# Optimization experiments

Hardware: AMD Instinct MI355X
Metric: run time of the kernel (lower is better)

The kernel has to match this reference:

```python
import jax, jax.numpy as jnp
import numpy as np

B, N, C_IN, C_H, C_OUT, R, X_DIM = 32, 256, 64, 128, 128, 5, 1024
NEG = -9e15

def _leaky(x, s=0.2):
    return jnp.where(x >= 0, x, s * x)

def gat_layer(atoms, mask, W, b, a):
    # atoms: (B,n,c_in), mask: (B,n,n,R) bool, W: (c_in, R*c), b: (R*c,), a: (R, 2c)
    bs, n, _ = atoms.shape
    c = a.shape[1] // 2
    h = (atoms @ W + b).reshape(bs, n, R, c)            # (B,n,R,c)
    src = jnp.einsum('bnrc,rc->bnr', h, a[:, :c])       # a . h_i part
    dst = jnp.einsum('bnrc,rc->bnr', h, a[:, c:])       # a . h_j part
    logits = _leaky(src[:, :, None, :] + dst[:, None, :, :])  # (B,i,j,R)
    masked = jnp.where(mask, logits, NEG)
    probs = jax.nn.softmax(masked.reshape(bs, n, n * R), axis=2).reshape(bs, n, n, R)
    return jnp.einsum('bijr,bjrc->bic', probs, h)       # (B,n,c)

def setup_inputs() -> dict:
    key = jax.random.key(0)
    ks = jax.random.split(key, 16)
    def p(k, shape, fan):
        return jax.random.normal(k, shape, jnp.float32) * (1.414 / np.sqrt(fan))
    inp = {
        'x': jax.random.normal(ks[0], (B, X_DIM), jnp.float32),
        'y_atoms': jax.random.normal(ks[1], (B, N, C_IN), jnp.float32),
        'y_bonds': jax.random.randint(ks[2], (B, N, N, R), 0, 2, jnp.int32),
        'W1': p(ks[3], (C_IN, R * C_H), C_IN), 'b1': jnp.zeros((R * C_H,), jnp.float32),
        'a1': p(ks[4], (R, 2 * C_H), 2 * C_H),
        'W2': p(ks[5], (C_H, R * C_H), C_H), 'b2': jnp.zeros((R * C_H,), jnp.float32),
        'a2': p(ks[6], (R, 2 * C_H), 2 * C_H),
        'W3': p(ks[7], (C_H, R * C_OUT), C_H), 'b3': jnp.zeros((R * C_OUT,), jnp.float32),
        'a3': p(ks[8], (R, 2 * C_OUT), 2 * C_OUT),
        'We1': p(ks[9], (2 * C_OUT + X_DIM, 256), 2 * C_OUT + X_DIM), 'be1': jnp.zeros((256,), jnp.float32),
        'We2': p(ks[10], (256, 32), 256), 'be2': jnp.zeros((32,), jnp.float32),
        'We3': p(ks[11], (32, 1), 32), 'be3': jnp.zeros((1,), jnp.float32),
    }
    return inp

def reference(x, y_atoms, y_bonds, W1, b1, a1, W2, b2, a2, W3, b3, a3,
              We1, be1, We2, be2, We3, be3):
    mask = (y_bonds == 1)
    h = gat_layer(y_atoms, mask, W1, b1, a1)
    h = _leaky(h)                                   # dropout is identity at eval
    h = gat_layer(h, mask, W2, b2, a2)
    h = _leaky(h)
    h = gat_layer(h, mask, W3, b3, a3)
    y_feats = jnp.concatenate([jnp.mean(h, axis=1), jnp.max(h, axis=1)], axis=1)
    z = jnp.concatenate([x, y_feats], axis=1)
    z = _leaky(z @ We1 + be1)
    z = _leaky(z @ We2 + be2)
    return z @ We3 + be3
```

## Files before the change

kernel.cpp:

```cpp
#include <hip/hip_runtime.h>
#include <cstddef>

#define NBLK 512

typedef __attribute__((ext_vector_type(8))) short bf16x8;
typedef __attribute__((ext_vector_type(4))) float f32x4;

__device__ __forceinline__ float lrelu(float x) { return x >= 0.f ? x : 0.2f * x; }
__device__ __forceinline__ unsigned short f2bf(float x) {
    unsigned u = __float_as_uint(x);
    u += 0x7FFFu + ((u >> 16) & 1u);
    return (unsigned short)(u >> 16);
}
__device__ __forceinline__ float bf2f(unsigned short u) {
    return __uint_as_float((unsigned)u << 16);
}

#define SY_CNT 0
#define SY_GA  256
#define SY_GR  512
#define SY_XB  1024
#define SY_XR  3072

__device__ __forceinline__ void xbar(unsigned* sync, int xcd, int r, unsigned cnt,
                                     unsigned ph, int t) {
    __syncthreads();
    if (t == 0) {
        __hip_atomic_fetch_add(&sync[SY_XB + (xcd * 8 + (r & 7)) * 32], 1u,
                               __ATOMIC_RELAXED, __HIP_MEMORY_SCOPE_AGENT);
        if (r == 0) {
            const unsigned tgt = cnt * ph;
            unsigned s;
            do {
                __builtin_amdgcn_s_sleep(2);
                s = 0;
#pragma unroll
                for (int i = 0; i < 8; ++i)
                    s += __hip_atomic_load(&sync[SY_XB + (xcd * 8 + i) * 32],
                                           __ATOMIC_RELAXED, __HIP_MEMORY_SCOPE_AGENT);
            } while (s < tgt);
            __hip_atomic_store(&sync[SY_XR + (xcd * 2 + 0) * 32], ph,
                               __ATOMIC_RELAXED, __HIP_MEMORY_SCOPE_AGENT);
            __hip_atomic_store(&sync[SY_XR + (xcd * 2 + 1) * 32], ph,
                               __ATOMIC_RELAXED, __HIP_MEMORY_SCOPE_AGENT);
        } else {
            unsigned* w = &sync[SY_XR + (xcd * 2 + (r & 1)) * 32];
            while (__hip_atomic_load(w, __ATOMIC_RELAXED, __HIP_MEMORY_SCOPE_AGENT) < ph)
                __builtin_amdgcn_s_sleep(16);
        }
    }
    __syncthreads();
}

__device__ __forceinline__ void wtrans(const float* __restrict__ W,
                                       unsigned short* __restrict__ WT,
                                       int K, int nt, int t) {
    int n = nt * 64 + (t & 63);
    for (int kg = t >> 6; kg < K / 8; kg += 8) {
        bf16x8 v;
#pragma unroll
        for (int e = 0; e < 8; ++e) v[e] = (short)f2bf(W[(size_t)(kg * 8 + e) * 640 + n]);
        *(bf16x8*)&WT[(size_t)n * K + kg * 8] = v;
    }
}

__device__ __forceinline__ void maskpack(const int* __restrict__ bonds,
                                         unsigned char* __restrict__ maskp, int gt) {
    const int4* p = (const int4*)(bonds + (size_t)gt * 20);
    int4 q0 = p[0], q1 = p[1], q2 = p[2], q3 = p[3], q4 = p[4];
    int v[20] = {q0.x, q0.y, q0.z, q0.w, q1.x, q1.y, q1.z, q1.w,
                 q2.x, q2.y, q2.z, q2.w, q3.x, q3.y, q3.z, q3.w,
                 q4.x, q4.y, q4.z, q4.w};
    unsigned m = 0;
#pragma unroll
    for (int k = 0; k < 4; ++k)
#pragma unroll
        for (int r = 0; r < 5; ++r)
            m |= (v[k * 5 + r] == 1) ? (1u << (k * 8 + r)) : 0u;
    *(unsigned*)&maskp[(size_t)gt * 4] = m;
}

template <int K, int MODE>
__device__ __forceinline__ void gemm_body(int mt, int nt, int t,
                                          const float* __restrict__ Af32,
                                          const unsigned short* __restrict__ Ab,
                                          const unsigned short* __restrict__ WTg,
                                          const float* __restrict__ bias,
                                          const float* __restrict__ avec,
                                          float* __restrict__ srcp,
                                          float* __restrict__ dstp,
                                          unsigned short* __restrict__ hTf) {
    const int n0 = nt * 64, m0 = mt * 64;
    const int w = t >> 6, lane = t & 63;
    const int colg = lane & 15, rquad = lane >> 4;
    const int m = m0 + w * 16 + colg;
    const int koff = rquad * 8;

    f32x4 acc[4] = {};
#pragma unroll
    for (int kk = 0; kk < K; kk += 32) {
        bf16x8 af;
        size_t off = (size_t)m * K + kk + koff;
        if (MODE == 1) {
            af = *(const bf16x8*)&Ab[off];
        } else {
            float4 q0 = *(const float4*)&Af32[off];
            float4 q1 = *(const float4*)&Af32[off + 4];
            af[0] = (short)f2bf(q0.x); af[1] = (short)f2bf(q0.y);
            af[2] = (short)f2bf(q0.z); af[3] = (short)f2bf(q0.w);
            af[4] = (short)f2bf(q1.x); af[5] = (short)f2bf(q1.y);
            af[6] = (short)f2bf(q1.z); af[7] = (short)f2bf(q1.w);
        }
#pragma unroll
        for (int ct = 0; ct < 4; ++ct) {
            bf16x8 bfv = *(const bf16x8*)&WTg[(size_t)(n0 + ct * 16 + colg) * K + kk + koff];
            acc[ct] = __builtin_amdgcn_mfma_f32_16x16x32_bf16(af, bfv, acc[ct], 0, 0, 0);
        }
    }

    const int r = n0 >> 7, chalf = n0 & 127;
    const int b = m0 >> 8, jb = m0 & 255;
    float val[4][4];
    float ssum[4] = {0.f, 0.f, 0.f, 0.f}, dsum[4] = {0.f, 0.f, 0.f, 0.f};
#pragma unroll
    for (int ct = 0; ct < 4; ++ct) {
        int cg = chalf + ct * 16 + colg;
        float bv = bias[n0 + ct * 16 + colg];
        float asr = avec[r * 256 + cg];
        float ads = avec[r * 256 + 128 + cg];
#pragma unroll
        for (int reg = 0; reg < 4; ++reg) {
            float v = acc[ct][reg] + bv;
            val[ct][reg] = v;
            ssum[reg] += v * asr;
            dsum[reg] += v * ads;
        }
    }
#pragma unroll
    for (int mk = 1; mk < 16; mk <<= 1)
#pragma unroll
        for (int reg = 0; reg < 4; ++reg) {
            ssum[reg] += __shfl_xor(ssum[reg], mk);
            dsum[reg] += __shfl_xor(dsum[reg], mk);
        }
    if (colg == 0) {
        int nhalf = (n0 >> 6) & 1;
#pragma unroll
        for (int reg = 0; reg < 4; ++reg) {
            int row = m0 + w * 16 + rquad * 4 + reg;
            srcp[nhalf * 40960 + row * 5 + r] = ssum[reg];
            dstp[nhalf * 40960 + row * 5 + r] = dsum[reg];
        }
    }
    {
        const int joct = (jb >> 3) + w * 2 + (rquad >> 1);
        const size_t tile = (size_t)((b * 5 + r) * 32 + joct) * 1024;
        const int sub = (rquad & 1) * 4;
#pragma unroll
        for (int ct = 0; ct < 4; ++ct) {
            int c = chalf + ct * 16 + colg;
            uint2 pk;
            pk.x = (unsigned)f2bf(val[ct][0]) | ((unsigned)f2bf(val[ct][1]) << 16);
            pk.y = (unsigned)f2bf(val[ct][2]) | ((unsigned)f2bf(val[ct][3]) << 16);
            *(uint2*)&hTf[tile + (size_t)c * 8 + sub] = pk;
        }
    }
}

template <int FINAL>
__device__ __forceinline__ void agg_body(int b, int itile, int t, unsigned char* SM,
                                         const unsigned short* __restrict__ hTf,
                                         const float* __restrict__ srcp,
                                         const float* __restrict__ dstp,
                                         const unsigned char* __restrict__ maskp,
                                         unsigned short* __restrict__ Ab,
                                         float* __restrict__ poolS,
                                         float* __restrict__ poolM) {
    unsigned short* Ps = (unsigned short*)SM;
    float* Ds2l = (float*)(SM + 40960);
    float* Ss   = (float*)(SM + 46080);
    float* Zw   = (float*)(SM + 46400);
    float* Zrow = (float*)(SM + 46912);

    const int ib = b * 256 + itile * 16;
    const int w = t >> 6, lane = t & 63;
    const int colg = lane & 15, rquad = lane >> 4;
    const int c = w * 16 + colg;
    const size_t bbase = (size_t)(b * 5) * 32 * 1024;

    if (t < 80) Ss[t] = srcp[(size_t)ib * 5 + t] + srcp[40960 + (size_t)ib * 5 + t];
    for (int idx = t; idx < 1280; idx += 512) {
        int jl = idx & 255, rr = idx >> 8;
        size_t o = (size_t)(b * 256 + jl) * 5 + rr;
        Ds2l[rr * 256 + jl] = dstp[o] + dstp[40960 + o];
    }
    bf16x8 pre[4];
#pragma unroll
    for (int s = 0; s < 4; ++s)
        pre[s] = *(const bf16x8*)&hTf[bbase + (size_t)(s * 4 + rquad) * 1024 + (size_t)c * 8];
    __syncthreads();

    {
        const int i = t & 15;
        const int kq = (t >> 4) & 3;
        float esum = 0.f;
#pragma unroll
        for (int it = 0; it < 5; ++it) {
            int p = it * 512 + t;
            int s = p >> 6;
            int k0 = s * 32 + kq * 8;
            int rr = k0 >> 8, j0 = k0 & 255;
            uint2 mk8 = *(const uint2*)&maskp[((size_t)(ib + i) << 8) + j0];
            float sv = Ss[i * 5 + rr];
            float4 d0 = *(const float4*)&Ds2l[rr * 256 + j0];
            float4 d1 = *(const float4*)&Ds2l[rr * 256 + j0 + 4];
            float dv[8] = {d0.x, d0.y, d0.z, d0.w, d1.x, d1.y, d1.z, d1.w};
            bf16x8 pv;
#pragma unroll
            for (int e = 0; e < 8; ++e) {
                unsigned mb = ((e < 4 ? (mk8.x >> (8 * e)) : (mk8.y >> (8 * (e - 4)))) >> rr) & 1u;
                float vv = lrelu(sv + dv[e]);
                float ev = mb ? __expf(vv) : 0.f;
                unsigned short q = f2bf(ev);
                pv[e] = (short)q;
                esum += __uint_as_float((unsigned)q << 16);
            }
            *(bf16x8*)&Ps[p * 8] = pv;
        }
        esum += __shfl_xor(esum, 16);
        esum += __shfl_xor(esum, 32);
        if (lane < 16) Zw[w * 16 + (lane & 15)] = esum;
    }
    __syncthreads();
    if (t < 16) {
        float z = 0.f;
#pragma unroll
        for (int ww = 0; ww < 8; ++ww) z += Zw[ww * 16 + t];
        Zrow[t] = 1.f / z;
    }

    f32x4 acc0 = {}, acc1 = {};
#pragma unroll
    for (int s = 0; s < 8; ++s) {
        bf16x8 af = *(const bf16x8*)&Ps[(s * 64 + lane) * 8];
        bf16x8 bfv;
        if (s < 4) bfv = pre[s];
        else bfv = *(const bf16x8*)&hTf[bbase + (size_t)((s & 7) * 4 + rquad) * 1024 + (size_t)c * 8];
        if (s & 1) acc1 = __builtin_amdgcn_mfma_f32_16x16x32_bf16(af, bfv, acc1, 0, 0, 0);
        else       acc0 = __builtin_amdgcn_mfma_f32_16x16x32_bf16(af, bfv, acc0, 0, 0, 0);
    }
#pragma unroll 8
    for (int s = 8; s < 40; ++s) {
        bf16x8 af = *(const bf16x8*)&Ps[(s * 64 + lane) * 8];
        bf16x8 bfv = *(const bf16x8*)&hTf[bbase +
            (size_t)((s >> 3) * 32 + (s & 7) * 4 + rquad) * 1024 + (size_t)c * 8];
        if (s & 1) acc1 = __builtin_amdgcn_mfma_f32_16x16x32_bf16(af, bfv, acc1, 0, 0, 0);
        else       acc0 = __builtin_amdgcn_mfma_f32_16x16x32_bf16(af, bfv, acc0, 0, 0, 0);
    }
    __syncthreads();
    const int irow = ib + rquad * 4;
    if (FINAL) {
        float ps = 0.f, pm = -3.4e38f;
#pragma unroll
        for (int reg = 0; reg < 4; ++reg) {
            float v = (acc0[reg] + acc1[reg]) * Zrow[rquad * 4 + reg];
            ps += v;
            pm = fmaxf(pm, v);
        }
        ps += __shfl_xor(ps, 16);
        ps += __shfl_xor(ps, 32);
        pm = fmaxf(pm, __shfl_xor(pm, 16));
        pm = fmaxf(pm, __shfl_xor(pm, 32));
        if (rquad == 0) {
            poolS[(size_t)(b * 16 + itile) * 128 + c] = ps;
            poolM[(size_t)(b * 16 + itile) * 128 + c] = pm;
        }
    } else {
#pragma unroll
        for (int reg = 0; reg < 4; ++reg) {
            float v = (acc0[reg] + acc1[reg]) * Zrow[rquad * 4 + reg];
            Ab[(size_t)(irow + reg) * 128 + c] = f2bf(lrelu(v));
        }
    }
}

__device__ __forceinline__ void mlp1_unit(int b, int kc, int t, float* zs,
                                          const float* __restrict__ x,
                                          const float* __restrict__ poolS,
                                          const float* __restrict__ poolM,
                                          const float* __restrict__ We1,
                                          float* __restrict__ z1p) {
    __syncthreads();
    if (t < 80) {
        int k = kc * 80 + t;
        float v;
        if (k < 1024) {
            v = x[(size_t)b * 1024 + k];
        } else if (k < 1152) {
            int f = k - 1024;
            float s = 0.f;
#pragma unroll
            for (int it = 0; it < 16; ++it) s += poolS[(size_t)(b * 16 + it) * 128 + f];
            v = s * (1.f / 256.f);
        } else {
            int f = k - 1152;
            float mx = -3.4e38f;
#pragma unroll
            for (int it = 0; it < 16; ++it) mx = fmaxf(mx, poolM[(size_t)(b * 16 + it) * 128 + f]);
            v = mx;
        }
        zs[t] = v;
    }
    __syncthreads();
    const int o = t & 255, half = t >> 8;
    float s = 0.f;
#pragma unroll 8
    for (int kk = 0; kk < 40; ++kk)
        s += zs[half * 40 + kk] * We1[(size_t)(kc * 80 + half * 40 + kk) * 256 + o];
    z1p[(size_t)(b * 16 + kc) * 512 + half * 256 + o] = s;
}

__device__ __forceinline__ void mlp2_body(int b, int t, unsigned char* SM,
                                          const float* __restrict__ z1p,
                                          const float* __restrict__ be1,
                                          const float* __restrict__ We2,
                                          const float* __restrict__ be2,
                                          const float* __restrict__ We3,
                                          const float* __restrict__ be3,
                                          float* __restrict__ out) {
    float* z1s = (float*)SM;
    float* s2p = (float*)(SM + 1024);
    float* z2s = (float*)(SM + 2048);
    if (t < 256) {
        float s = be1[t];
#pragma unroll
        for (int kc = 0; kc < 16; ++kc) {
            size_t base = (size_t)(b * 16 + kc) * 512;
            s += z1p[base + t] + z1p[base + 256 + t];
        }
        z1s[t] = lrelu(s);
    }
    __syncthreads();
    if (t < 256) {
        int o = t & 31, g = t >> 5;
        float p = 0.f;
#pragma unroll
        for (int k = 0; k < 32; ++k) p += z1s[g * 32 + k] * We2[(g * 32 + k) * 32 + o];
        s2p[g * 32 + o] = p;
    }
    __syncthreads();
    if (t < 32) {
        float s2 = be2[t];
#pragma unroll
        for (int g = 0; g < 8; ++g) s2 += s2p[g * 32 + t];
        z2s[t] = lrelu(s2);
    }
    __syncthreads();
    if (t == 0) {
        float s3 = be3[0];
#pragma unroll
        for (int k = 0; k < 32; ++k) s3 += z2s[k] * We3[k];
        out[b] = s3;
    }
}

constexpr size_t O_MASK  = 0;
constexpr size_t O_SRC   = 2097152;  constexpr size_t SRC_SZ = 327680;
constexpr size_t O_DST   = O_SRC + 3 * SRC_SZ;
constexpr size_t O_AB    = O_DST + 3 * SRC_SZ;  constexpr size_t AB_SZ = 2097152;
constexpr size_t O_HT    = O_AB + 2 * AB_SZ;    constexpr size_t HT_SZ = 10485760;
constexpr size_t O_WTX   = O_HT + 3 * HT_SZ;    constexpr size_t WTX_SZ = 409600;
constexpr size_t O_POOLS = O_WTX + 8 * WTX_SZ;
constexpr size_t O_POOLM = O_POOLS + 262144;
constexpr size_t O_Z1P   = O_POOLM + 262144;
constexpr size_t O_SYNC  = O_Z1P + 1048576;

__global__ __launch_bounds__(512, 4) void k_mega(
    const float* __restrict__ x, const float* __restrict__ y_atoms,
    const int* __restrict__ bonds,
    const float* __restrict__ W1, const float* __restrict__ b1, const float* __restrict__ a1,
    const float* __restrict__ W2, const float* __restrict__ b2, const float* __restrict__ a2,
    const float* __restrict__ W3, const float* __restrict__ b3, const float* __restrict__ a3,
    const float* __restrict__ We1, const float* __restrict__ be1,
    const float* __restrict__ We2, const float* __restrict__ be2,
    const float* __restrict__ We3, const float* __restrict__ be3,
    char* __restrict__ ws, float* __restrict__ out) {
    __shared__ __align__(16) unsigned char SM[46976];
    __shared__ unsigned s_nfo[3];
    const int rb = blockIdx.x;
    const int t = threadIdx.x;
    const int hb = t >> 8, t2 = t & 255;

    unsigned char* maskp = (unsigned char*)(ws + O_MASK);
    unsigned* sync = (unsigned*)(ws + O_SYNC);
    float* poolS = (float*)(ws + O_POOLS);
    float* poolM = (float*)(ws + O_POOLM);
    float* z1p   = (float*)(ws + O_Z1P);

    if (t == 0) {
        unsigned xr;
        asm volatile("s_getreg_b32 %0, hwreg(HW_REG_XCC_ID)" : "=s"(xr));
        xr &= 7u;
        unsigned rk = __hip_atomic_fetch_add(&sync[SY_CNT + xr * 32], 1u,
                                             __ATOMIC_RELAXED, __HIP_MEMORY_SCOPE_AGENT);
        __hip_atomic_fetch_add(&sync[SY_GA + (rb & 7) * 32], 1u,
                               __ATOMIC_RELAXED, __HIP_MEMORY_SCOPE_AGENT);
        if (rb == 0) {
            unsigned s;
            do {
                __builtin_amdgcn_s_sleep(2);
                s = 0;
#pragma unroll
                for (int i = 0; i < 8; ++i)
                    s += __hip_atomic_load(&sync[SY_GA + i * 32],
                                           __ATOMIC_RELAXED, __HIP_MEMORY_SCOPE_AGENT);
            } while (s < NBLK);
#pragma unroll
            for (int g = 0; g < 16; ++g)
                __hip_atomic_store(&sync[SY_GR + g * 32], 1u,
                                   __ATOMIC_RELAXED, __HIP_MEMORY_SCOPE_AGENT);
        } else {
            unsigned* w = &sync[SY_GR + (rb >> 5) * 32];
            while (__hip_atomic_load(w, __ATOMIC_RELAXED, __HIP_MEMORY_SCOPE_AGENT) < 1u)
                __builtin_amdgcn_s_sleep(16);
        }
        s_nfo[0] = xr;
        s_nfo[1] = rk;
        s_nfo[2] = __hip_atomic_load(&sync[SY_CNT + xr * 32],
                                     __ATOMIC_RELAXED, __HIP_MEMORY_SCOPE_AGENT);
    }
    __syncthreads();
    const int xcd = (int)s_nfo[0];
    const int r = (int)s_nfo[1];
    const unsigned cnt = s_nfo[2];

    unsigned short* WT1x = (unsigned short*)(ws + O_WTX + (size_t)xcd * WTX_SZ);
    unsigned short* WT2x = WT1x + 40960;
    unsigned short* WT3x = WT2x + 81920;
    float* src0 = (float*)(ws + O_SRC);
    float* src1 = (float*)(ws + O_SRC + SRC_SZ);
    float* src2 = (float*)(ws + O_SRC + 2 * SRC_SZ);
    float* dst0 = (float*)(ws + O_DST);
    float* dst1 = (float*)(ws + O_DST + SRC_SZ);
    float* dst2 = (float*)(ws + O_DST + 2 * SRC_SZ);
    unsigned short* Ab0 = (unsigned short*)(ws + O_AB);
    unsigned short* Ab1 = (unsigned short*)(ws + O_AB + AB_SZ);
    unsigned short* hT0 = (unsigned short*)(ws + O_HT);
    unsigned short* hT1 = (unsigned short*)(ws + O_HT + HT_SZ);
    unsigned short* hT2 = (unsigned short*)(ws + O_HT + 2 * HT_SZ);

    for (int u = r; u < 10; u += cnt) wtrans(W1, WT1x, 64, u, t);
    xbar(sync, xcd, r, cnt, 1, t);

    for (int u = r; u < 20; u += cnt) {
        if (u < 10) wtrans(W2, WT2x, 128, u, t);
        else        wtrans(W3, WT3x, 128, u - 10, t);
    }
    for (int u = 2 * r + hb; u < 160; u += 2 * cnt) {
        int b = xcd + (u & 3) * 8;
        int mt = b * 4 + ((u >> 2) & 3), nt = u >> 4;
        gemm_body<64, 0>(mt, nt, t2, y_atoms, nullptr, WT1x, b1, a1, src0, dst0, hT0);
    }
    for (unsigned u = r * 512u + t; u < 65536u; u += cnt * 512u) {
        int b = xcd + (int)(u >> 14) * 8;
        maskpack(bonds, maskp, b * 16384 + (int)(u & 16383u));
    }
    xbar(sync, xcd, r, cnt, 2, t);

    for (int u = r; u < 64; u += cnt)
        agg_body<0>(xcd + (u & 3) * 8, u >> 2, t, SM, hT0, src0, dst0, maskp,
                    Ab0, nullptr, nullptr);
    xbar(sync, xcd, r, cnt, 3, t);

    for (int u = 2 * r + hb; u < 160; u += 2 * cnt) {
        int b = xcd + (u & 3) * 8;
        int mt = b * 4 + ((u >> 2) & 3), nt = u >> 4;
        gemm_body<128, 1>(mt, nt, t2, nullptr, Ab0, WT2x, b2, a2, src1, dst1, hT1);
    }
    xbar(sync, xcd, r, cnt, 4, t);

    for (int u = r; u < 64; u += cnt)
        agg_body<0>(xcd + (u & 3) * 8, u >> 2, t, SM, hT1, src1, dst1, maskp,
                    Ab1, nullptr, nullptr);
    xbar(sync, xcd, r, cnt, 5, t);

    for (int u = 2 * r + hb; u < 160; u += 2 * cnt) {
        int b = xcd + (u & 3) * 8;
        int mt = b * 4 + ((u >> 2) & 3), nt = u >> 4;
        gemm_body<128, 1>(mt, nt, t2, nullptr, Ab1, WT3x, b3, a3, src2, dst2, hT2);
    }
    xbar(sync, xcd, r, cnt, 6, t);

    for (int u = r; u < 64; u += cnt)
        agg_body<1>(xcd + (u & 3) * 8, u >> 2, t, SM, hT2, src2, dst2, maskp,
                    nullptr, poolS, poolM);
    xbar(sync, xcd, r, cnt, 7, t);

    for (int u = r; u < 64; u += cnt)
        mlp1_unit(xcd + (u & 3) * 8, u >> 2, t, (float*)SM, x, poolS, poolM, We1, z1p);
    xbar(sync, xcd, r, cnt, 8, t);

    for (int u = r; u < 4; u += cnt)
        mlp2_body(xcd + u * 8, t, SM, z1p, be1, We2, be2, We3, be3, out);
}

extern "C" void kernel_launch(void* const* d_in, const int* in_sizes, int n_in,
                              void* d_out, int out_size, void* d_ws, size_t ws_size,
                              hipStream_t stream) {
    const float* x       = (const float*)d_in[0];
    const float* y_atoms = (const float*)d_in[1];
    const int*   y_bonds = (const int*)d_in[2];
    const float* W1 = (const float*)d_in[3];
    const float* b1 = (const float*)d_in[4];
    const float* a1 = (const float*)d_in[5];
    const float* W2 = (const float*)d_in[6];
    const float* b2 = (const float*)d_in[7];
    const float* a2 = (const float*)d_in[8];
    const float* W3 = (const float*)d_in[9];
    const float* b3 = (const float*)d_in[10];
    const float* a3 = (const float*)d_in[11];
    const float* We1 = (const float*)d_in[12];
    const float* be1 = (const float*)d_in[13];
    const float* We2 = (const float*)d_in[14];
    const float* be2 = (const float*)d_in[15];
    const float* We3 = (const float*)d_in[16];
    const float* be3 = (const float*)d_in[17];
    float* out = (float*)d_out;
    char* ws = (char*)d_ws;

    hipMemsetAsync(ws + O_SYNC, 0, 16384, stream);
    k_mega<<<NBLK, 512, 0, stream>>>(
        x, y_atoms, y_bonds, W1, b1, a1, W2, b2, a2, W3, b3, a3,
        We1, be1, We2, be2, We3, be3, ws, out);
}
```

Before: 219.2 us.

## Remove barriers by fusing MLP stages, front-loading weight prep, and batching loads

Moves weight transposition and mask packing ahead of the grid-wide start barrier so they overlap with block arrival, which drops one cross-block barrier. The two MLP stages are fused into a single per-batch body that keeps its partial sums in shared memory, removing another barrier and the z1p workspace. The GEMM and aggregation loops now load operands in batches before issuing MFMAs, and the mask loads are hoisted. The release flags in the barrier are spread over four lines and the sleep intervals are shortened. In exchange, the MLP1 work runs on only 4 blocks per XCD instead of being spread across blocks, and a fallback path redoes all the prep work when the block count is not 64.

Result: slower. 244.2 us (+11.4%).

```diff
diff --git a/kernel.cpp b/kernel.cpp
--- a/kernel.cpp
+++ b/kernel.cpp
@@ -32,21 +32,21 @@
             const unsigned tgt = cnt * ph;
             unsigned s;
             do {
-                __builtin_amdgcn_s_sleep(2);
+                __builtin_amdgcn_s_sleep(1);
                 s = 0;
 #pragma unroll
                 for (int i = 0; i < 8; ++i)
                     s += __hip_atomic_load(&sync[SY_XB + (xcd * 8 + i) * 32],
                                            __ATOMIC_RELAXED, __HIP_MEMORY_SCOPE_AGENT);
             } while (s < tgt);
-            __hip_atomic_store(&sync[SY_XR + (xcd * 2 + 0) * 32], ph,
-                               __ATOMIC_RELAXED, __HIP_MEMORY_SCOPE_AGENT);
-            __hip_atomic_store(&sync[SY_XR + (xcd * 2 + 1) * 32], ph,
-                               __ATOMIC_RELAXED, __HIP_MEMORY_SCOPE_AGENT);
+#pragma unroll
+            for (int g = 0; g < 4; ++g)
+                __hip_atomic_store(&sync[SY_XR + (xcd * 4 + g) * 32], ph,
+                                   __ATOMIC_RELAXED, __HIP_MEMORY_SCOPE_AGENT);
         } else {
-            unsigned* w = &sync[SY_XR + (xcd * 2 + (r & 1)) * 32];
+            unsigned* w = &sync[SY_XR + (xcd * 4 + (r & 3)) * 32];
             while (__hip_atomic_load(w, __ATOMIC_RELAXED, __HIP_MEMORY_SCOPE_AGENT) < ph)
-                __builtin_amdgcn_s_sleep(16);
+                __builtin_amdgcn_s_sleep(8);
         }
     }
     __syncthreads();
@@ -96,26 +96,35 @@
     const int m = m0 + w * 16 + colg;
     const int koff = rquad * 8;
 
-    f32x4 acc[4] = {};
+    bf16x8 afr[K / 32];
 #pragma unroll
     for (int kk = 0; kk < K; kk += 32) {
-        bf16x8 af;
         size_t off = (size_t)m * K + kk + koff;
         if (MODE == 1) {
-            af = *(const bf16x8*)&Ab[off];
+            afr[kk >> 5] = *(const bf16x8*)&Ab[off];
         } else {
             float4 q0 = *(const float4*)&Af32[off];
             float4 q1 = *(const float4*)&Af32[off + 4];
+            bf16x8 af;
             af[0] = (short)f2bf(q0.x); af[1] = (short)f2bf(q0.y);
             af[2] = (short)f2bf(q0.z); af[3] = (short)f2bf(q0.w);
             af[4] = (short)f2bf(q1.x); af[5] = (short)f2bf(q1.y);
             af[6] = (short)f2bf(q1.z); af[7] = (short)f2bf(q1.w);
-        }
-#pragma unroll
-        for (int ct = 0; ct < 4; ++ct) {
-            bf16x8 bfv = *(const bf16x8*)&WTg[(size_t)(n0 + ct * 16 + colg) * K + kk + koff];
-            acc[ct] = __builtin_amdgcn_mfma_f32_16x16x32_bf16(af, bfv, acc[ct], 0, 0, 0);
-        }
+            afr[kk >> 5] = af;
+        }
+    }
+    f32x4 acc[4] = {};
+#pragma unroll
+    for (int kk = 0; kk < K; kk += 32) {
+        bf16x8 af = afr[kk >> 5];
+        bf16x8 b0 = *(const bf16x8*)&WTg[(size_t)(n0 + 0 * 16 + colg) * K + kk + koff];
+        bf16x8 b1 = *(const bf16x8*)&WTg[(size_t)(n0 + 1 * 16 + colg) * K + kk + koff];
+        bf16x8 b2 = *(const bf16x8*)&WTg[(size_t)(n0 + 2 * 16 + colg) * K + kk + koff];
+        bf16x8 b3 = *(const bf16x8*)&WTg[(size_t)(n0 + 3 * 16 + colg) * K + kk + koff];
+        acc[0] = __builtin_amdgcn_mfma_f32_16x16x32_bf16(af, b0, acc[0], 0, 0, 0);
+        acc[1] = __builtin_amdgcn_mfma_f32_16x16x32_bf16(af, b1, acc[1], 0, 0, 0);
+        acc[2] = __builtin_amdgcn_mfma_f32_16x16x32_bf16(af, b2, acc[2], 0, 0, 0);
+        acc[3] = __builtin_amdgcn_mfma_f32_16x16x32_bf16(af, b3, acc[3], 0, 0, 0);
     }
 
     const int r = n0 >> 7, chalf = n0 & 127;
@@ -203,6 +212,14 @@
     {
         const int i = t & 15;
         const int kq = (t >> 4) & 3;
+        uint2 mk[5];
+#pragma unroll
+        for (int it = 0; it < 5; ++it) {
+            int p = it * 512 + t;
+            int s = p >> 6;
+            int k0 = s * 32 + kq * 8;
+            mk[it] = *(const uint2*)&maskp[((size_t)(ib + i) << 8) + (k0 & 255)];
+        }
         float esum = 0.f;
 #pragma unroll
         for (int it = 0; it < 5; ++it) {
@@ -210,7 +227,7 @@
             int s = p >> 6;
             int k0 = s * 32 + kq * 8;
             int rr = k0 >> 8, j0 = k0 & 255;
-            uint2 mk8 = *(const uint2*)&maskp[((size_t)(ib + i) << 8) + j0];
+            uint2 mk8 = mk[it];
             float sv = Ss[i * 5 + rr];
             float4 d0 = *(const float4*)&Ds2l[rr * 256 + j0];
             float4 d1 = *(const float4*)&Ds2l[rr * 256 + j0 + 4];
@@ -241,21 +258,40 @@
 
     f32x4 acc0 = {}, acc1 = {};
 #pragma unroll
-    for (int s = 0; s < 8; ++s) {
+    for (int s = 0; s < 4; ++s) {
         bf16x8 af = *(const bf16x8*)&Ps[(s * 64 + lane) * 8];
-        bf16x8 bfv;
-        if (s < 4) bfv = pre[s];
-        else bfv = *(const bf16x8*)&hTf[bbase + (size_t)((s & 7) * 4 + rquad) * 1024 + (size_t)c * 8];
-        if (s & 1) acc1 = __builtin_amdgcn_mfma_f32_16x16x32_bf16(af, bfv, acc1, 0, 0, 0);
-        else       acc0 = __builtin_amdgcn_mfma_f32_16x16x32_bf16(af, bfv, acc0, 0, 0, 0);
-    }
-#pragma unroll 8
-    for (int s = 8; s < 40; ++s) {
-        bf16x8 af = *(const bf16x8*)&Ps[(s * 64 + lane) * 8];
-        bf16x8 bfv = *(const bf16x8*)&hTf[bbase +
-            (size_t)((s >> 3) * 32 + (s & 7) * 4 + rquad) * 1024 + (size_t)c * 8];
-        if (s & 1) acc1 = __builtin_amdgcn_mfma_f32_16x16x32_bf16(af, bfv, acc1, 0, 0, 0);
-        else       acc0 = __builtin_amdgcn_mfma_f32_16x16x32_bf16(af, bfv, acc0, 0, 0, 0);
+        if (s & 1) acc1 = __builtin_amdgcn_mfma_f32_16x16x32_bf16(af, pre[s], acc1, 0, 0, 0);
+        else       acc0 = __builtin_amdgcn_mfma_f32_16x16x32_bf16(af, pre[s], acc0, 0, 0, 0);
+    }
+    {
+        bf16x8 aq[4], bq[4];
+#pragma unroll
+        for (int q = 0; q < 4; ++q) {
+            int s = 4 + q;
+            aq[q] = *(const bf16x8*)&Ps[(s * 64 + lane) * 8];
+            bq[q] = *(const bf16x8*)&hTf[bbase +
+                (size_t)((s >> 3) * 32 + (s & 7) * 4 + rquad) * 1024 + (size_t)c * 8];
+        }
+#pragma unroll
+        for (int q = 0; q < 4; ++q) {
+            if (q & 1) acc1 = __builtin_amdgcn_mfma_f32_16x16x32_bf16(aq[q], bq[q], acc1, 0, 0, 0);
+            else       acc0 = __builtin_amdgcn_mfma_f32_16x16x32_bf16(aq[q], bq[q], acc0, 0, 0, 0);
+        }
+    }
+    for (int s8 = 8; s8 < 40; s8 += 8) {
+        bf16x8 aq[8], bq[8];
+#pragma unroll
+        for (int q = 0; q < 8; ++q) {
+            int s = s8 + q;
+            aq[q] = *(const bf16x8*)&Ps[(s * 64 + lane) * 8];
+            bq[q] = *(const bf16x8*)&hTf[bbase +
+                (size_t)((s >> 3) * 32 + (s & 7) * 4 + rquad) * 1024 + (size_t)c * 8];
+        }
+#pragma unroll
+        for (int q = 0; q < 8; ++q) {
+            if (q & 1) acc1 = __builtin_amdgcn_mfma_f32_16x16x32_bf16(aq[q], bq[q], acc1, 0, 0, 0);
+            else       acc0 = __builtin_amdgcn_mfma_f32_16x16x32_bf16(aq[q], bq[q], acc0, 0, 0, 0);
+        }
     }
     __syncthreads();
     const int irow = ib + rquad * 4;
@@ -284,15 +320,24 @@
     }
 }
 
-__device__ __forceinline__ void mlp1_unit(int b, int kc, int t, float* zs,
+__device__ __forceinline__ void mlp_fused(int b, int t, unsigned char* SM,
                                           const float* __restrict__ x,
                                           const float* __restrict__ poolS,
                                           const float* __restrict__ poolM,
                                           const float* __restrict__ We1,
-                                          float* __restrict__ z1p) {
-    __syncthreads();
-    if (t < 80) {
-        int k = kc * 80 + t;
+                                          const float* __restrict__ be1,
+                                          const float* __restrict__ We2,
+                                          const float* __restrict__ be2,
+                                          const float* __restrict__ We3,
+                                          const float* __restrict__ be3,
+                                          float* __restrict__ out) {
+    float* zs  = (float*)SM;
+    float* p16 = (float*)(SM + 5120);
+    float* z1s = (float*)(SM + 37888);
+    float* s2p = (float*)(SM + 38912);
+    float* z2s = (float*)(SM + 39936);
+    __syncthreads();
+    for (int k = t; k < 1280; k += 512) {
         float v;
         if (k < 1024) {
             v = x[(size_t)b * 1024 + k];
@@ -309,44 +354,33 @@
             for (int it = 0; it < 16; ++it) mx = fmaxf(mx, poolM[(size_t)(b * 16 + it) * 128 + f]);
             v = mx;
         }
-        zs[t] = v;
+        zs[k] = v;
     }
     __syncthreads();
     const int o = t & 255, half = t >> 8;
-    float s = 0.f;
+#pragma unroll
+    for (int kc = 0; kc < 16; ++kc) {
+        float s = 0.f;
 #pragma unroll 8
-    for (int kk = 0; kk < 40; ++kk)
-        s += zs[half * 40 + kk] * We1[(size_t)(kc * 80 + half * 40 + kk) * 256 + o];
-    z1p[(size_t)(b * 16 + kc) * 512 + half * 256 + o] = s;
-}
-
-__device__ __forceinline__ void mlp2_body(int b, int t, unsigned char* SM,
-                                          const float* __restrict__ z1p,
-                                          const float* __restrict__ be1,
-                                          const float* __restrict__ We2,
-                                          const float* __restrict__ be2,
-                                          const float* __restrict__ We3,
-                                          const float* __restrict__ be3,
-                                          float* __restrict__ out) {
-    float* z1s = (float*)SM;
-    float* s2p = (float*)(SM + 1024);
-    float* z2s = (float*)(SM + 2048);
+        for (int kk = 0; kk < 40; ++kk)
+            s += zs[kc * 80 + half * 40 + kk] * We1[(size_t)(kc * 80 + half * 40 + kk) * 256 + o];
+        p16[kc * 512 + half * 256 + o] = s;
+    }
+    __syncthreads();
     if (t < 256) {
         float s = be1[t];
 #pragma unroll
-        for (int kc = 0; kc < 16; ++kc) {
-            size_t base = (size_t)(b * 16 + kc) * 512;
-            s += z1p[base + t] + z1p[base + 256 + t];
-        }
+        for (int kc = 0; kc < 16; ++kc)
+            s += p16[kc * 512 + t] + p16[kc * 512 + 256 + t];
         z1s[t] = lrelu(s);
     }
     __syncthreads();
     if (t < 256) {
-        int o = t & 31, g = t >> 5;
+        int oo = t & 31, g = t >> 5;
         float p = 0.f;
 #pragma unroll
-        for (int k = 0; k < 32; ++k) p += z1s[g * 32 + k] * We2[(g * 32 + k) * 32 + o];
-        s2p[g * 32 + o] = p;
+        for (int k = 0; k < 32; ++k) p += z1s[g * 32 + k] * We2[(g * 32 + k) * 32 + oo];
+        s2p[g * 32 + oo] = p;
     }
     __syncthreads();
     if (t < 32) {
@@ -372,8 +406,7 @@
 constexpr size_t O_WTX   = O_HT + 3 * HT_SZ;    constexpr size_t WTX_SZ = 409600;
 constexpr size_t O_POOLS = O_WTX + 8 * WTX_SZ;
 constexpr size_t O_POOLM = O_POOLS + 262144;
-constexpr size_t O_Z1P   = O_POOLM + 262144;
-constexpr size_t O_SYNC  = O_Z1P + 1048576;
+constexpr size_t O_SYNC  = O_POOLM + 262144;
 
 __global__ __launch_bounds__(512, 4) void k_mega(
     const float* __restrict__ x, const float* __restrict__ y_atoms,
@@ -395,7 +428,6 @@
     unsigned* sync = (unsigned*)(ws + O_SYNC);
     float* poolS = (float*)(ws + O_POOLS);
     float* poolM = (float*)(ws + O_POOLM);
-    float* z1p   = (float*)(ws + O_Z1P);
 
     if (t == 0) {
         unsigned xr;
@@ -403,12 +435,33 @@
         xr &= 7u;
         unsigned rk = __hip_atomic_fetch_add(&sync[SY_CNT + xr * 32], 1u,
                                              __ATOMIC_RELAXED, __HIP_MEMORY_SCOPE_AGENT);
+        s_nfo[0] = xr;
+        s_nfo[1] = rk;
+    }
+    __syncthreads();
+    const int xcd = (int)s_nfo[0];
+    const int r0 = (int)s_nfo[1];
+
+    unsigned short* WT1x = (unsigned short*)(ws + O_WTX + (size_t)xcd * WTX_SZ);
+    unsigned short* WT2x = WT1x + 40960;
+    unsigned short* WT3x = WT2x + 81920;
+
+    if (r0 < 10)      wtrans(W1, WT1x, 64, r0, t);
+    else if (r0 < 20) wtrans(W2, WT2x, 128, r0 - 10, t);
+    else if (r0 < 30) wtrans(W3, WT3x, 128, r0 - 20, t);
+    for (unsigned u = (unsigned)r0 * 512u + t; u < 65536u; u += 64u * 512u) {
+        int b = xcd + (int)(u >> 14) * 8;
+        maskpack(bonds, maskp, b * 16384 + (int)(u & 16383u));
+    }
+    __syncthreads();
+
+    if (t == 0) {
         __hip_atomic_fetch_add(&sync[SY_GA + (rb & 7) * 32], 1u,
                                __ATOMIC_RELAXED, __HIP_MEMORY_SCOPE_AGENT);
         if (rb == 0) {
             unsigned s;
             do {
-                __builtin_amdgcn_s_sleep(2);
+                __builtin_amdgcn_s_sleep(1);
                 s = 0;
 #pragma unroll
                 for (int i = 0; i < 8; ++i)
@@ -422,21 +475,14 @@
         } else {
             unsigned* w = &sync[SY_GR + (rb >> 5) * 32];
             while (__hip_atomic_load(w, __ATOMIC_RELAXED, __HIP_MEMORY_SCOPE_AGENT) < 1u)
-                __builtin_amdgcn_s_sleep(16);
-        }
-        s_nfo[0] = xr;
-        s_nfo[1] = rk;
-        s_nfo[2] = __hip_atomic_load(&sync[SY_CNT + xr * 32],
+                __builtin_amdgcn_s_sleep(8);
+        }
+        s_nfo[2] = __hip_atomic_load(&sync[SY_CNT + xcd * 32],
                                      __ATOMIC_RELAXED, __HIP_MEMORY_SCOPE_AGENT);
     }
     __syncthreads();
-    const int xcd = (int)s_nfo[0];
-    const int r = (int)s_nfo[1];
     const unsigned cnt = s_nfo[2];
 
-    unsigned short* WT1x = (unsigned short*)(ws + O_WTX + (size_t)xcd * WTX_SZ);
-    unsigned short* WT2x = WT1x + 40960;
-    unsigned short* WT3x = WT2x + 81920;
     float* src0 = (float*)(ws + O_SRC);
     float* src1 = (float*)(ws + O_SRC + SRC_SZ);
     float* src2 = (float*)(ws + O_SRC + 2 * SRC_SZ);
@@ -449,59 +495,54 @@
     unsigned short* hT1 = (unsigned short*)(ws + O_HT + HT_SZ);
     unsigned short* hT2 = (unsigned short*)(ws + O_HT + 2 * HT_SZ);
 
-    for (int u = r; u < 10; u += cnt) wtrans(W1, WT1x, 64, u, t);
-    xbar(sync, xcd, r, cnt, 1, t);
-
-    for (int u = r; u < 20; u += cnt) {
-        if (u < 10) wtrans(W2, WT2x, 128, u, t);
-        else        wtrans(W3, WT3x, 128, u - 10, t);
-    }
-    for (int u = 2 * r + hb; u < 160; u += 2 * cnt) {
+    if (cnt != 64u) {
+        for (int u = 0; u < 10; ++u) wtrans(W1, WT1x, 64, u, t);
+        for (int u = 0; u < 10; ++u) wtrans(W2, WT2x, 128, u, t);
+        for (int u = 0; u < 10; ++u) wtrans(W3, WT3x, 128, u, t);
+        __syncthreads();
+        for (unsigned u = t; u < 65536u; u += 512u) {
+            int b = xcd + (int)(u >> 14) * 8;
+            maskpack(bonds, maskp, b * 16384 + (int)(u & 16383u));
+        }
+    }
+    for (int u = 2 * r0 + hb; u < 160; u += 2 * (int)cnt) {
         int b = xcd + (u & 3) * 8;
         int mt = b * 4 + ((u >> 2) & 3), nt = u >> 4;
         gemm_body<64, 0>(mt, nt, t2, y_atoms, nullptr, WT1x, b1, a1, src0, dst0, hT0);
     }
-    for (unsigned u = r * 512u + t; u < 65536u; u += cnt * 512u) {
-        int b = xcd + (int)(u >> 14) * 8;
-        maskpack(bonds, maskp, b * 16384 + (int)(u & 16383u));
-    }
-    xbar(sync, xcd, r, cnt, 2, t);
-
-    for (int u = r; u < 64; u += cnt)
+    xbar(sync, xcd, r0, cnt, 1, t);
+
+    for (int u = r0; u < 64; u += (int)cnt)
         agg_body<0>(xcd + (u & 3) * 8, u >> 2, t, SM, hT0, src0, dst0, maskp,
                     Ab0, nullptr, nullptr);
-    xbar(sync, xcd, r, cnt, 3, t);
-
-    for (int u = 2 * r + hb; u < 160; u += 2 * cnt) {
+    xbar(sync, xcd, r0, cnt, 2, t);
+
+    for (int u = 2 * r0 + hb; u < 160; u += 2 * (int)cnt) {
         int b = xcd + (u & 3) * 8;
         int mt = b * 4 + ((u >> 2) & 3), nt = u >> 4;
         gemm_body<128, 1>(mt, nt, t2, nullptr, Ab0, WT2x, b2, a2, src1, dst1, hT1);
     }
-    xbar(sync, xcd, r, cnt, 4, t);
-
-    for (int u = r; u < 64; u += cnt)
+    xbar(sync, xcd, r0, cnt, 3, t);
+
+    for (int u = r0; u < 64; u += (int)cnt)
         agg_body<0>(xcd + (u & 3) * 8, u >> 2, t, SM, hT1, src1, dst1, maskp,
                     Ab1, nullptr, nullptr);
-    xbar(sync, xcd, r, cnt, 5, t);
-
-    for (int u = 2 * r + hb; u < 160; u += 2 * cnt) {
+    xbar(sync, xcd, r0, cnt, 4, t);
+
+    for (int u = 2 * r0 + hb; u < 160; u += 2 * (int)cnt) {
         int b = xcd + (u & 3) * 8;
         int mt = b * 4 + ((u >> 2) & 3), nt = u >> 4;
         gemm_body<128, 1>(mt, nt, t2, nullptr, Ab1, WT3x, b3, a3, src2, dst2, hT2);
     }
-    xbar(sync, xcd, r, cnt, 6, t);
-
-    for (int u = r; u < 64; u += cnt)
+    xbar(sync, xcd, r0, cnt, 5, t);
+
+    for (int u = r0; u < 64; u += (int)cnt)
         agg_body<1>(xcd + (u & 3) * 8, u >> 2, t, SM, hT2, src2, dst2, maskp,
                     nullptr, poolS, poolM);
-    xbar(sync, xcd, r, cnt, 7, t);
-
-    for (int u = r; u < 64; u += cnt)
-        mlp1_unit(xcd + (u & 3) * 8, u >> 2, t, (float*)SM, x, poolS, poolM, We1, z1p);
-    xbar(sync, xcd, r, cnt, 8, t);
-
-    for (int u = r; u < 4; u += cnt)
-        mlp2_body(xcd + u * 8, t, SM, z1p, be1, We2, be2, We3, be3, out);
+    xbar(sync, xcd, r0, cnt, 6, t);
+
+    for (int u = r0; u < 4; u += (int)cnt)
+        mlp_fused(xcd + u * 8, t, SM, x, poolS, poolM, We1, be1, We2, be2, We3, be3, out);
 }
 
 extern "C" void kernel_launch(void* const* d_in, const int* in_sizes, int n_in,
```
